# Performance work log

Hardware: AMD Instinct MI355X
Metric: run time of the kernel (lower is better)

The kernel has to match this reference:

```python
import jax, jax.numpy as jnp
import numpy as np

N_NODES, N_EDGES = 50000, 150000
HEADS, OUT = 2, 325


def _lin(k, i, o):
    return (jax.random.normal(k, (i, o), jnp.float32) / np.float32(np.sqrt(i)))


def setup_inputs() -> dict:
    key = jax.random.key(0)
    ks = jax.random.split(key, 24)
    h = jax.random.normal(ks[0], (N_NODES, 5), jnp.float32)
    edge_num = jax.random.normal(ks[1], (N_NODES, 5), jnp.float32)
    edge_index = jax.random.randint(ks[2], (2, N_EDGES), 0, N_NODES)
    edge_weight = jax.random.uniform(ks[3], (N_EDGES,), jnp.float32)
    d = dict(h=h, edge_num=edge_num, edge_index=edge_index, edge_weight=edge_weight)
    # five GCNConv layers: weight [5,64], bias [64]
    names = ['sum', 'mean', 'max', 'ne', 'nem']
    for i, nm in enumerate(names):
        d['W_' + nm] = _lin(ks[4 + i], 5, 64)
        d['b_' + nm] = jnp.zeros((64,), jnp.float32)
    # GATv2Conv params
    d['Wl'] = _lin(ks[10], 325, HEADS * OUT)
    d['Wr'] = _lin(ks[11], 325, HEADS * OUT)
    d['We'] = _lin(ks[12], 1, HEADS * OUT)
    d['att'] = jax.random.normal(ks[13], (HEADS, OUT), jnp.float32) / np.float32(np.sqrt(OUT))
    d['b_att'] = jnp.zeros((OUT,), jnp.float32)
    d['W_fc1'] = _lin(ks[14], 325, 5)
    d['b_fc1'] = jnp.zeros((5,), jnp.float32)
    return d


def _seg_mean(m, idx, n):
    s = jax.ops.segment_sum(m, idx, n)
    c = jax.ops.segment_sum(jnp.ones((m.shape[0],), m.dtype), idx, n)
    return s / jnp.clip(c, 1.0)[:, None]


def _seg_max0(m, idx, n):
    o = jax.ops.segment_max(m, idx, n)
    return jnp.where(jnp.isfinite(o), o, jnp.zeros_like(o))  # empty segments -> 0 (PyG behavior)


def _gcn(x, W, b, src, dst, w, aggr, n):
    # GCNConv(normalize=False, add_self_loops=False): aggr_j w_ij * (x_j @ W) + b
    m = (x @ W)[src]
    if w is not None:
        m = m * w[:, None]
    if aggr == 'add':
        o = jax.ops.segment_sum(m, dst, n)
    elif aggr == 'mean':
        o = _seg_mean(m, dst, n)
    else:
        o = _seg_max0(m, dst, n)
    return o + b


def _forward(h, edge_num, edge_weight, W_sum, b_sum, W_mean, b_mean, W_max, b_max,
             W_ne, b_ne, W_nem, b_nem, Wl, Wr, We, att, b_att, W_fc1, b_fc1, edge_index):
    n = h.shape[0]
    src, dst = edge_index[0], edge_index[1]
    h1 = _gcn(h, W_sum, b_sum, src, dst, edge_weight, 'add', n)
    h2 = _gcn(h, W_mean, b_mean, src, dst, edge_weight, 'mean', n)
    h3 = _gcn(h, W_max, b_max, src, dst, edge_weight, 'max', n)
    h4 = _gcn(h, W_ne, b_ne, src, dst, None, 'add', n)
    h5 = _gcn(h, W_nem, b_nem, src, dst, None, 'max', n)
    x = jnp.concatenate([h1, h2, h3, h4, h5, edge_num], axis=-1)  # [N, 325]
    # GATv2Conv(heads=2, concat=False, aggr='mean', add_self_loops=True, fill_value='mean')
    loop = jnp.arange(n)
    src2 = jnp.concatenate([src, loop])
    dst2 = jnp.concatenate([dst, loop])
    ea = jnp.concatenate([edge_weight[:, None], jnp.full((n, 1), jnp.mean(edge_weight))], axis=0)
    xl = (x @ Wl).reshape(n, HEADS, OUT)  # source transform
    xr = (x @ Wr).reshape(n, HEADS, OUT)  # target transform
    ee = (ea @ We).reshape(-1, HEADS, OUT)
    f = jax.nn.leaky_relu(xl[src2] + xr[dst2] + ee, 0.2)  # [E2, H, C]
    alpha = jnp.einsum('ehc,hc->eh', f, att)
    mx = jax.ops.segment_max(alpha, dst2, n)
    a = jnp.exp(alpha - mx[dst2])
    a = a / jax.ops.segment_sum(a, dst2, n)[dst2]  # softmax over incoming edges
    msg = xl[src2] * a[:, :, None]
    cnt = jax.ops.segment_sum(jnp.ones((src2.shape[0],), x.dtype), dst2, n)
    agg = jax.ops.segment_sum(msg, dst2, n) / jnp.clip(cnt, 1.0)[:, None, None]  # aggr='mean'
    o = agg.mean(axis=1) + b_att  # concat=False -> head mean
    return o @ W_fc1 + b_fc1


def reference(h, edge_num, edge_index, edge_weight, W_sum, b_sum, W_mean, b_mean,
              W_max, b_max, W_ne, b_ne, W_nem, b_nem, Wl, Wr, We, att, b_att,
              W_fc1, b_fc1):
    return _forward(h, edge_num, edge_weight, W_sum, b_sum, W_mean, b_mean, W_max, b_max,
                    W_ne, b_ne, W_nem, b_nem, Wl, Wr, We, att, b_att, W_fc1, b_fc1, edge_index)
```

## Files before the change

kernel.cpp:

```cpp
#include <hip/hip_runtime.h>
#include <hip/hip_bf16.h>
#include <math.h>

#define N_NODES 50000
#define N_EDGES 150000
#define FDIM 325
#define KP 352
#define HCP 1312
#define XROFF 656
#define LDA 40
#define LDC 136
#define NPAN 391
#define NBJ 11
#define SCAN_B 256
#define NBLK ((N_NODES + SCAN_B - 1) / SCAN_B)

typedef unsigned short ushort_t;
typedef __attribute__((ext_vector_type(8))) short short8v;
typedef __attribute__((ext_vector_type(4))) float f32x4;

__device__ __forceinline__ float bf2f(ushort_t u) {
  return __uint_as_float(((unsigned)u) << 16);
}
__device__ __forceinline__ ushort_t f2bf(float f) {
  __hip_bfloat16 h = __float2bfloat16(f);
  union { __hip_bfloat16 h; ushort_t u; } cv; cv.h = h;
  return cv.u;
}

__global__ void k_init(int* deg, int* cursor, float* red) {
  int i = blockIdx.x * blockDim.x + threadIdx.x;
  if (i < N_NODES) { deg[i] = 0; cursor[i] = 0; }
  if (i == 0) red[0] = 0.f;
}

__global__ void k_count(const int* __restrict__ dst, const float* __restrict__ ew,
                        int* deg, float* red) {
  int e = blockIdx.x * blockDim.x + threadIdx.x;
  float w = 0.f;
  if (e < N_EDGES) { atomicAdd(&deg[dst[e]], 1); w = ew[e]; }
  #pragma unroll
  for (int m = 32; m; m >>= 1) w += __shfl_xor(w, m);
  if ((threadIdx.x & 63) == 0) atomicAdd(red, w);
}

__global__ void k_scan1(const int* __restrict__ deg, int* offs, int* bsum) {
  __shared__ int buf[SCAN_B];
  int b = blockIdx.x, tid = threadIdx.x, i = b * SCAN_B + tid;
  int v = (i < N_NODES) ? deg[i] : 0;
  buf[tid] = v;
  __syncthreads();
  for (int o = 1; o < SCAN_B; o <<= 1) {
    int t = (tid >= o) ? buf[tid - o] : 0;
    __syncthreads();
    buf[tid] += t;
    __syncthreads();
  }
  if (i < N_NODES) offs[i + 1] = buf[tid];
  if (tid == SCAN_B - 1) bsum[b] = buf[tid];
}
__global__ void k_scan2(const int* __restrict__ bsum, int* bofs) {
  __shared__ int buf[256];
  int tid = threadIdx.x;
  int v = (tid < NBLK) ? bsum[tid] : 0;
  buf[tid] = v;
  __syncthreads();
  for (int o = 1; o < 256; o <<= 1) {
    int t = (tid >= o) ? buf[tid - o] : 0;
    __syncthreads();
    buf[tid] += t;
    __syncthreads();
  }
  if (tid < NBLK) bofs[tid] = buf[tid] - v;
}
__global__ void k_scan3(const int* __restrict__ bofs, int* offs) {
  int i = blockIdx.x * blockDim.x + threadIdx.x;
  if (i == 0) offs[0] = 0;
  if (i < N_NODES) offs[i + 1] += bofs[i / SCAN_B];
}

__global__ void k_scatter(const int* __restrict__ src, const int* __restrict__ dst,
                          const float* __restrict__ ew, const int* __restrict__ offs,
                          int* cursor, int* csr_src, float* csr_w) {
  int e = blockIdx.x * blockDim.x + threadIdx.x;
  if (e >= N_EDGES) return;
  int d = dst[e];
  int p = offs[d] + atomicAdd(&cursor[d], 1);
  csr_src[p] = src[e];
  csr_w[p] = ew[e];
}

__global__ void __launch_bounds__(64) k_gcn(
    const float* __restrict__ h, const float* __restrict__ edge_num,
    const int* __restrict__ offs, const int* __restrict__ csr_src,
    const float* __restrict__ csr_w,
    const float* __restrict__ Wsum, const float* __restrict__ bsum,
    const float* __restrict__ Wmean, const float* __restrict__ bmean,
    const float* __restrict__ Wmax, const float* __restrict__ bmax,
    const float* __restrict__ Wne, const float* __restrict__ bne,
    const float* __restrict__ Wnem, const float* __restrict__ bnem,
    ushort_t* __restrict__ x) {
  int n = blockIdx.x;
  int t = threadIdx.x;
  float w0[5], w1[5], w2[5], w3[5], w4[5];
  #pragma unroll
  for (int k = 0; k < 5; ++k) {
    w0[k] = Wsum[k * 64 + t];
    w1[k] = Wmean[k * 64 + t];
    w2[k] = Wmax[k * 64 + t];
    w3[k] = Wne[k * 64 + t];
    w4[k] = Wnem[k * 64 + t];
  }
  float s_sum = 0.f, s_wmean = 0.f, s_max = -INFINITY, s_ne = 0.f, s_nem = -INFINITY;
  int beg = offs[n], end = offs[n + 1];
  float wcur = 0.f, hcur[5];
  if (beg < end) {
    int s = csr_src[beg];
    wcur = csr_w[beg];
    #pragma unroll
    for (int k = 0; k < 5; ++k) hcur[k] = h[s * 5 + k];
  }
  for (int i = beg; i < end; ++i) {
    float wnxt = 0.f, hnxt[5];
    if (i + 1 < end) {
      int s = csr_src[i + 1];
      wnxt = csr_w[i + 1];
      #pragma unroll
      for (int k = 0; k < 5; ++k) hnxt[k] = h[s * 5 + k];
    }
    float v0 = 0, v1 = 0, v2 = 0, v3 = 0, v4 = 0;
    #pragma unroll
    for (int k = 0; k < 5; ++k) {
      v0 += hcur[k] * w0[k]; v1 += hcur[k] * w1[k]; v2 += hcur[k] * w2[k];
      v3 += hcur[k] * w3[k]; v4 += hcur[k] * w4[k];
    }
    s_sum += wcur * v0;
    s_wmean += wcur * v1;
    s_max = fmaxf(s_max, wcur * v2);
    s_ne += v3;
    s_nem = fmaxf(s_nem, v4);
    wcur = wnxt;
    #pragma unroll
    for (int k = 0; k < 5; ++k) hcur[k] = hnxt[k];
  }
  int dg = end - beg;
  float inv = 1.f / (float)(dg > 0 ? dg : 1);
  ushort_t* xr = x + (size_t)n * KP;
  xr[t]       = f2bf(s_sum + bsum[t]);
  xr[64 + t]  = f2bf(s_wmean * inv + bmean[t]);
  xr[128 + t] = f2bf((dg ? s_max : 0.f) + bmax[t]);
  xr[192 + t] = f2bf(s_ne + bne[t]);
  xr[256 + t] = f2bf((dg ? s_nem : 0.f) + bnem[t]);
  if (t < 5) xr[320 + t] = f2bf(edge_num[n * 5 + t]);
  if (t < KP - FDIM) xr[FDIM + t] = 0;
}

__global__ void k_wt(const float* __restrict__ Wl, const float* __restrict__ Wr,
                     ushort_t* __restrict__ Wt) {
  int t = blockIdx.x * blockDim.x + threadIdx.x;
  if (t >= HCP * KP) return;
  int n = t / KP, k = t % KP;
  float v = 0.f;
  if (k < FDIM) {
    if (n < 650) v = Wl[(size_t)k * 650 + n];
    else if (n >= XROFF && n < XROFF + 650) v = Wr[(size_t)k * 650 + (n - XROFF)];
  }
  Wt[t] = f2bf(v);
}

__global__ void __launch_bounds__(256) k_gemm_mfma(
    const ushort_t* __restrict__ x, const ushort_t* __restrict__ Wt,
    ushort_t* __restrict__ xlr) {
  __shared__ ushort_t smem[128 * LDA * 2];
  ushort_t* As = smem;
  ushort_t* Bs = smem + 128 * LDA;
  ushort_t* Cs = smem;

  int L = blockIdx.x;
  int panel, jb;
  if (L < 4224) {
    int chunk = L / 88, g = L % 88;
    panel = chunk * 8 + (g & 7);
    jb = g >> 3;
  } else {
    int g = L - 4224;
    panel = 384 + g % 7;
    jb = g / 7;
  }
  int bm = panel * 128, bn = jb * 128;

  int tid = threadIdx.x;
  int lane = tid & 63, wave = tid >> 6;
  int wr = wave >> 1, wc = wave & 1;
  int srow = tid >> 2, skc = (tid & 3) << 3;
  const float4 fz = make_float4(0.f, 0.f, 0.f, 0.f);

  float4 pa0, pa1, pb0, pb1;
  {
    int gm0 = bm + srow, gm1 = gm0 + 64;
    int gn0 = bn + srow, gn1 = gn0 + 64;
    pa0 = (gm0 < N_NODES) ? *(const float4*)&x[(size_t)gm0 * KP + skc] : fz;
    pa1 = (gm1 < N_NODES) ? *(const float4*)&x[(size_t)gm1 * KP + skc] : fz;
    pb0 = (gn0 < HCP)     ? *(const float4*)&Wt[(size_t)gn0 * KP + skc] : fz;
    pb1 = (gn1 < HCP)     ? *(const float4*)&Wt[(size_t)gn1 * KP + skc] : fz;
  }
  f32x4 acc[4][4] = {};
  for (int k0 = 0; k0 < KP; k0 += 32) {
    *(float4*)&As[srow * LDA + skc]        = pa0;
    *(float4*)&As[(srow + 64) * LDA + skc] = pa1;
    *(float4*)&Bs[srow * LDA + skc]        = pb0;
    *(float4*)&Bs[(srow + 64) * LDA + skc] = pb1;
    __syncthreads();
    int kn = k0 + 32;
    if (kn < KP) {
      int gm0 = bm + srow, gm1 = gm0 + 64;
      int gn0 = bn + srow, gn1 = gn0 + 64;
      pa0 = (gm0 < N_NODES) ? *(const float4*)&x[(size_t)gm0 * KP + kn + skc] : fz;
      pa1 = (gm1 < N_NODES) ? *(const float4*)&x[(size_t)gm1 * KP + kn + skc] : fz;
      pb0 = (gn0 < HCP)     ? *(const float4*)&Wt[(size_t)gn0 * KP + kn + skc] : fz;
      pb1 = (gn1 < HCP)     ? *(const float4*)&Wt[(size_t)gn1 * KP + kn + skc] : fz;
    }
    int koff = (lane >> 4) << 3;
    int ar = (wr << 6) + (lane & 15);
    int br = (wc << 6) + (lane & 15);
    short8v a[4], b[4];
    #pragma unroll
    for (int i = 0; i < 4; ++i) a[i] = *(const short8v*)&As[(ar + i * 16) * LDA + koff];
    #pragma unroll
    for (int j = 0; j < 4; ++j) b[j] = *(const short8v*)&Bs[(br + j * 16) * LDA + koff];
    #pragma unroll
    for (int i = 0; i < 4; ++i)
      #pragma unroll
      for (int j = 0; j < 4; ++j)
        acc[i][j] = __builtin_amdgcn_mfma_f32_16x16x32_bf16(a[i], b[j], acc[i][j], 0, 0, 0);
    __syncthreads();
  }
  #pragma unroll
  for (int half = 0; half < 2; ++half) {
    if (wr == half) {
      int lr0 = ((lane >> 4) << 2);
      int c0 = (wc << 6) + (lane & 15);
      #pragma unroll
      for (int i = 0; i < 4; ++i)
        #pragma unroll
        for (int j = 0; j < 4; ++j)
          #pragma unroll
          for (int r = 0; r < 4; ++r)
            Cs[(lr0 + i * 16 + r) * LDC + c0 + j * 16] = f2bf(acc[i][j][r]);
    }
    __syncthreads();
    #pragma unroll
    for (int it = 0; it < 4; ++it) {
      int idx = tid + it * 256;
      int lr = idx >> 4, cc = idx & 15;
      int row = bm + half * 64 + lr;
      int col = bn + cc * 8;
      if (row < N_NODES && col < HCP) {
        short8v v = *(const short8v*)&Cs[lr * LDC + cc * 8];
        *(short8v*)&xlr[(size_t)row * HCP + col] = v;
      }
    }
    __syncthreads();
  }
}

__global__ void k_wlf(const float* __restrict__ Wl, const float* __restrict__ Wfc,
                      float* __restrict__ Wlf) {
  int t = blockIdx.x * blockDim.x + threadIdx.x;
  if (t >= FDIM * 10) return;
  int cp = t / 10, o = t % 10;
  int hh = o / 5, j = o % 5;
  float s = 0.f;
  for (int c = 0; c < 325; ++c) s += Wl[(size_t)cp * 650 + hh * 325 + c] * Wfc[c * 5 + j];
  Wlf[cp * 10 + o] = s;
}

__global__ void k_yl(const ushort_t* __restrict__ x, const float* __restrict__ Wlf,
                     float* __restrict__ yl) {
  int wid = (blockIdx.x * blockDim.x + threadIdx.x) >> 6;
  int lane = threadIdx.x & 63;
  if (wid >= N_NODES) return;
  const ushort_t* row = x + (size_t)wid * KP;
  float p[10] = {};
  for (int c = lane; c < FDIM; c += 64) {
    float v = bf2f(row[c]);
    const float* wr = Wlf + c * 10;
    #pragma unroll
    for (int j = 0; j < 10; ++j) p[j] += v * wr[j];
  }
  #pragma unroll
  for (int j = 0; j < 10; ++j)
    #pragma unroll
    for (int m = 32; m; m >>= 1) p[j] += __shfl_xor(p[j], m);
  if (lane == 0) {
    #pragma unroll
    for (int j = 0; j < 10; ++j) yl[(size_t)wid * 10 + j] = p[j];
  }
}

__global__ void k_cvec(const float* __restrict__ b_att, const float* __restrict__ Wfc,
                       const float* __restrict__ b_fc1, const float* __restrict__ red,
                       float* __restrict__ cvec) {
  int j = threadIdx.x;
  if (j == 5) cvec[5] = red[0] / (float)N_EDGES;
  if (j < 5) {
    float s = b_fc1[j];
    for (int c = 0; c < 325; ++c) s += b_att[c] * Wfc[c * 5 + j];
    cvec[j] = s;
  }
}

__global__ void __launch_bounds__(64) k_att(
    const int* __restrict__ offs, const int* __restrict__ csrs,
    const float* __restrict__ csrw, const ushort_t* __restrict__ xlr,
    const float* __restrict__ We, const float* __restrict__ att,
    const float* __restrict__ cvec, const float* __restrict__ yl,
    float* __restrict__ out) {
  int d = blockIdx.x;
  int lane = threadIdx.x;
  float xd0[8], xd1[8], We0[8], We1[8], at0[8], at1[8];
  const ushort_t* xd = xlr + (size_t)d * HCP + XROFF;
  {
    short8v v = *(const short8v*)&xd[lane * 8];
    int c0 = lane * 8;
    #pragma unroll
    for (int e = 0; e < 8; ++e) {
      xd0[e] = bf2f((ushort_t)v[e]);
      We0[e] = We[c0 + e];
      at0[e] = att[c0 + e];
    }
  }
  if (lane < 18) {
    short8v v = *(const short8v*)&xd[512 + lane * 8];
    int c0 = 512 + lane * 8;
    #pragma unroll
    for (int e = 0; e < 8; ++e) {
      bool ok = (c0 + e) < 650;
      xd1[e] = bf2f((ushort_t)v[e]);
      We1[e] = ok ? We[c0 + e] : 0.f;
      at1[e] = ok ? att[c0 + e] : 0.f;
    }
  }
  float meanw = cvec[5];
  int beg = offs[d], end = offs[d + 1];
  float m0 = -INFINITY, m1 = -INFINITY, s0 = 0.f, s1 = 0.f;
  float oj = 0.f;

  float ea_c, yv_c = 0.f;
  short8v v0_c, v1_c;
  {
    int s;
    if (beg < end) { s = csrs[beg]; ea_c = csrw[beg]; }
    else { s = d; ea_c = meanw; }
    const ushort_t* xs = xlr + (size_t)s * HCP;
    v0_c = *(const short8v*)&xs[lane * 8];
    if (lane < 18) v1_c = *(const short8v*)&xs[512 + lane * 8];
    if (lane < 10) yv_c = yl[(size_t)s * 10 + lane];
  }
  for (int i = beg; i <= end; ++i) {
    float ea_n = 0.f, yv_n = 0.f;
    short8v v0_n, v1_n;
    bool have_next = (i < end);
    if (have_next) {
      int s;
      if (i + 1 < end) { s = csrs[i + 1]; ea_n = csrw[i + 1]; }
      else { s = d; ea_n = meanw; }
      const ushort_t* xs = xlr + (size_t)s * HCP;
      v0_n = *(const short8v*)&xs[lane * 8];
      if (lane < 18) v1_n = *(const short8v*)&xs[512 + lane * 8];
      if (lane < 10) yv_n = yl[(size_t)s * 10 + lane];
    }
    float p0 = 0.f, p1 = 0.f;
    {
      int c0 = lane * 8;
      #pragma unroll
      for (int e = 0; e < 8; ++e) {
        float vv = bf2f((ushort_t)v0_c[e]) + xd0[e] + ea_c * We0[e];
        vv = (vv > 0.f) ? vv : 0.2f * vv;
        float t = vv * at0[e];
        if (c0 + e < 325) p0 += t; else p1 += t;
      }
    }
    if (lane < 18) {
      #pragma unroll
      for (int e = 0; e < 8; ++e) {
        float vv = bf2f((ushort_t)v1_c[e]) + xd1[e] + ea_c * We1[e];
        vv = (vv > 0.f) ? vv : 0.2f * vv;
        p1 += vv * at1[e];
      }
    }
    #pragma unroll
    for (int m = 32; m; m >>= 1) { p0 += __shfl_xor(p0, m); p1 += __shfl_xor(p1, m); }
    float nm0 = fmaxf(m0, p0), nm1 = fmaxf(m1, p1);
    float r0 = __expf(m0 - nm0), r1 = __expf(m1 - nm1);
    float e0 = __expf(p0 - nm0), e1 = __expf(p1 - nm1);
    s0 = s0 * r0 + e0; s1 = s1 * r1 + e1;
    m0 = nm0; m1 = nm1;
    if (lane < 10) {
      float r = (lane < 5) ? r0 : r1;
      float e = (lane < 5) ? e0 : e1;
      oj = oj * r + e * yv_c;
    }
    if (have_next) { ea_c = ea_n; yv_c = yv_n; v0_c = v0_n; v1_c = v1_n; }
  }
  float on = oj / ((lane < 5) ? s0 : s1);
  float other = __shfl(on, lane + 5);
  if (lane < 5) {
    int dg = end - beg;
    out[(size_t)d * 5 + lane] = (on + other) / (2.f * (float)(dg + 1)) + cvec[lane];
  }
}

extern "C" void kernel_launch(void* const* d_in, const int* in_sizes, int n_in,
                              void* d_out, int out_size, void* d_ws, size_t ws_size,
                              hipStream_t stream) {
  (void)in_sizes; (void)n_in; (void)out_size; (void)ws_size;
  const float* h        = (const float*)d_in[0];
  const float* edge_num = (const float*)d_in[1];
  const int*   eidx     = (const int*)d_in[2];
  const float* ew       = (const float*)d_in[3];
  const float* Wsum  = (const float*)d_in[4];  const float* bsum_  = (const float*)d_in[5];
  const float* Wmean = (const float*)d_in[6];  const float* bmean = (const float*)d_in[7];
  const float* Wmax  = (const float*)d_in[8];  const float* bmax  = (const float*)d_in[9];
  const float* Wne   = (const float*)d_in[10]; const float* bne   = (const float*)d_in[11];
  const float* Wnem  = (const float*)d_in[12]; const float* bnem  = (const float*)d_in[13];
  const float* Wl    = (const float*)d_in[14]; const float* Wr    = (const float*)d_in[15];
  const float* We    = (const float*)d_in[16]; const float* att   = (const float*)d_in[17];
  const float* b_att = (const float*)d_in[18];
  const float* Wfc   = (const float*)d_in[19]; const float* bfc   = (const float*)d_in[20];
  const int* src = eidx;
  const int* dst = eidx + N_EDGES;
  float* out = (float*)d_out;

  char* p = (char*)d_ws;
  size_t off = 0;
  auto alloc = [&](size_t bytes) { char* r = p + off; off = (off + bytes + 255) & ~(size_t)255; return r; };
  ushort_t* x   = (ushort_t*)alloc((size_t)N_NODES * KP * 2);
  ushort_t* xlr = (ushort_t*)alloc((size_t)N_NODES * HCP * 2);
  ushort_t* Wt  = (ushort_t*)alloc((size_t)HCP * KP * 2);
  float* yl     = (float*)alloc((size_t)N_NODES * 10 * 4);
  int*   deg    = (int*)alloc((size_t)N_NODES * 4);
  int*   offs   = (int*)alloc((size_t)(N_NODES + 1) * 4);
  int*   cursor = (int*)alloc((size_t)N_NODES * 4);
  int*   csrs   = (int*)alloc((size_t)N_EDGES * 4);
  float* csrw   = (float*)alloc((size_t)N_EDGES * 4);
  int*   bsum   = (int*)alloc((size_t)NBLK * 4);
  int*   bofs   = (int*)alloc((size_t)NBLK * 4);
  float* Wlf    = (float*)alloc((size_t)FDIM * 10 * 4);
  float* red    = (float*)alloc(64);
  float* cvec   = (float*)alloc(64);

  k_init<<<(N_NODES + 255) / 256, 256, 0, stream>>>(deg, cursor, red);
  k_count<<<(N_EDGES + 255) / 256, 256, 0, stream>>>(dst, ew, deg, red);
  k_scan1<<<NBLK, SCAN_B, 0, stream>>>(deg, offs, bsum);
  k_scan2<<<1, 256, 0, stream>>>(bsum, bofs);
  k_scan3<<<NBLK, SCAN_B, 0, stream>>>(bofs, offs);
  k_scatter<<<(N_EDGES + 255) / 256, 256, 0, stream>>>(src, dst, ew, offs, cursor, csrs, csrw);
  k_gcn<<<N_NODES, 64, 0, stream>>>(h, edge_num, offs, csrs, csrw,
                                    Wsum, bsum_, Wmean, bmean, Wmax, bmax,
                                    Wne, bne, Wnem, bnem, x);
  k_wt<<<(HCP * KP + 255) / 256, 256, 0, stream>>>(Wl, Wr, Wt);
  k_gemm_mfma<<<NPAN * NBJ, 256, 0, stream>>>(x, Wt, xlr);
  k_wlf<<<(FDIM * 10 + 255) / 256, 256, 0, stream>>>(Wl, Wfc, Wlf);
  k_yl<<<(N_NODES * 64 + 255) / 256, 256, 0, stream>>>(x, Wlf, yl);
  k_cvec<<<1, 64, 0, stream>>>(b_att, Wfc, bfc, red, cvec);
  k_att<<<N_NODES, 64, 0, stream>>>(offs, csrs, csrw, xlr, We, att, cvec, yl, out);
}
```

Baseline: 410.4 us.

## Use persistent waves with atomic work counter for GCN and attention kernels

Replaces the one-block-per-node launches of the GCN aggregation and GATv2 attention kernels with a fixed grid of 256-thread blocks. Each wavefront repeatedly claims a destination node through a global atomic counter. Per-wave constants (weights, biases, attention vectors) are now loaded once and reused across many nodes. This is meant to cut block launch/scheduling overhead and balance degree skew, at the cost of one atomic per node and two extra counters to reset.

```diff
diff --git a/kernel.cpp b/kernel.cpp
--- a/kernel.cpp
+++ b/kernel.cpp
@@ -28,10 +28,10 @@
   return cv.u;
 }
 
-__global__ void k_init(int* deg, int* cursor, float* red) {
+__global__ void k_init(int* deg, int* cursor, float* red, int* wc1, int* wc2) {
   int i = blockIdx.x * blockDim.x + threadIdx.x;
   if (i < N_NODES) { deg[i] = 0; cursor[i] = 0; }
-  if (i == 0) red[0] = 0.f;
+  if (i == 0) { red[0] = 0.f; wc1[0] = 0; wc2[0] = 0; }
 }
 
 __global__ void k_count(const int* __restrict__ dst, const float* __restrict__ ew,
@@ -90,7 +90,7 @@
   csr_w[p] = ew[e];
 }
 
-__global__ void __launch_bounds__(64) k_gcn(
+__global__ void __launch_bounds__(256) k_gcn(
     const float* __restrict__ h, const float* __restrict__ edge_num,
     const int* __restrict__ offs, const int* __restrict__ csr_src,
     const float* __restrict__ csr_w,
@@ -99,9 +99,8 @@
     const float* __restrict__ Wmax, const float* __restrict__ bmax,
     const float* __restrict__ Wne, const float* __restrict__ bne,
     const float* __restrict__ Wnem, const float* __restrict__ bnem,
-    ushort_t* __restrict__ x) {
-  int n = blockIdx.x;
-  int t = threadIdx.x;
+    ushort_t* __restrict__ x, int* __restrict__ workc) {
+  int t = threadIdx.x & 63;
   float w0[5], w1[5], w2[5], w3[5], w4[5];
   #pragma unroll
   for (int k = 0; k < 5; ++k) {
@@ -111,48 +110,55 @@
     w3[k] = Wne[k * 64 + t];
     w4[k] = Wnem[k * 64 + t];
   }
-  float s_sum = 0.f, s_wmean = 0.f, s_max = -INFINITY, s_ne = 0.f, s_nem = -INFINITY;
-  int beg = offs[n], end = offs[n + 1];
-  float wcur = 0.f, hcur[5];
-  if (beg < end) {
-    int s = csr_src[beg];
-    wcur = csr_w[beg];
-    #pragma unroll
-    for (int k = 0; k < 5; ++k) hcur[k] = h[s * 5 + k];
-  }
-  for (int i = beg; i < end; ++i) {
-    float wnxt = 0.f, hnxt[5];
-    if (i + 1 < end) {
-      int s = csr_src[i + 1];
-      wnxt = csr_w[i + 1];
-      #pragma unroll
-      for (int k = 0; k < 5; ++k) hnxt[k] = h[s * 5 + k];
-    }
-    float v0 = 0, v1 = 0, v2 = 0, v3 = 0, v4 = 0;
-    #pragma unroll
-    for (int k = 0; k < 5; ++k) {
-      v0 += hcur[k] * w0[k]; v1 += hcur[k] * w1[k]; v2 += hcur[k] * w2[k];
-      v3 += hcur[k] * w3[k]; v4 += hcur[k] * w4[k];
-    }
-    s_sum += wcur * v0;
-    s_wmean += wcur * v1;
-    s_max = fmaxf(s_max, wcur * v2);
-    s_ne += v3;
-    s_nem = fmaxf(s_nem, v4);
-    wcur = wnxt;
-    #pragma unroll
-    for (int k = 0; k < 5; ++k) hcur[k] = hnxt[k];
-  }
-  int dg = end - beg;
-  float inv = 1.f / (float)(dg > 0 ? dg : 1);
-  ushort_t* xr = x + (size_t)n * KP;
-  xr[t]       = f2bf(s_sum + bsum[t]);
-  xr[64 + t]  = f2bf(s_wmean * inv + bmean[t]);
-  xr[128 + t] = f2bf((dg ? s_max : 0.f) + bmax[t]);
-  xr[192 + t] = f2bf(s_ne + bne[t]);
-  xr[256 + t] = f2bf((dg ? s_nem : 0.f) + bnem[t]);
-  if (t < 5) xr[320 + t] = f2bf(edge_num[n * 5 + t]);
-  if (t < KP - FDIM) xr[FDIM + t] = 0;
+  float b0 = bsum[t], b1 = bmean[t], b2 = bmax[t], b3 = bne[t], b4 = bnem[t];
+  for (;;) {
+    int n;
+    if (t == 0) n = atomicAdd(workc, 1);
+    n = __shfl(n, 0);
+    if (n >= N_NODES) break;
+    float s_sum = 0.f, s_wmean = 0.f, s_max = -INFINITY, s_ne = 0.f, s_nem = -INFINITY;
+    int beg = offs[n], end = offs[n + 1];
+    float wcur = 0.f, hcur[5];
+    if (beg < end) {
+      int s = csr_src[beg];
+      wcur = csr_w[beg];
+      #pragma unroll
+      for (int k = 0; k < 5; ++k) hcur[k] = h[s * 5 + k];
+    }
+    for (int i = beg; i < end; ++i) {
+      float wnxt = 0.f, hnxt[5];
+      if (i + 1 < end) {
+        int s = csr_src[i + 1];
+        wnxt = csr_w[i + 1];
+        #pragma unroll
+        for (int k = 0; k < 5; ++k) hnxt[k] = h[s * 5 + k];
+      }
+      float v0 = 0, v1 = 0, v2 = 0, v3 = 0, v4 = 0;
+      #pragma unroll
+      for (int k = 0; k < 5; ++k) {
+        v0 += hcur[k] * w0[k]; v1 += hcur[k] * w1[k]; v2 += hcur[k] * w2[k];
+        v3 += hcur[k] * w3[k]; v4 += hcur[k] * w4[k];
+      }
+      s_sum += wcur * v0;
+      s_wmean += wcur * v1;
+      s_max = fmaxf(s_max, wcur * v2);
+      s_ne += v3;
+      s_nem = fmaxf(s_nem, v4);
+      wcur = wnxt;
+      #pragma unroll
+      for (int k = 0; k < 5; ++k) hcur[k] = hnxt[k];
+    }
+    int dg = end - beg;
+    float inv = 1.f / (float)(dg > 0 ? dg : 1);
+    ushort_t* xr = x + (size_t)n * KP;
+    xr[t]       = f2bf(s_sum + b0);
+    xr[64 + t]  = f2bf(s_wmean * inv + b1);
+    xr[128 + t] = f2bf((dg ? s_max : 0.f) + b2);
+    xr[192 + t] = f2bf(s_ne + b3);
+    xr[256 + t] = f2bf((dg ? s_nem : 0.f) + b4);
+    if (t < 5) xr[320 + t] = f2bf(edge_num[n * 5 + t]);
+    if (t < KP - FDIM) xr[FDIM + t] = 0;
+  }
 }
 
 __global__ void k_wt(const float* __restrict__ Wl, const float* __restrict__ Wr,
@@ -310,104 +316,116 @@
   }
 }
 
-__global__ void __launch_bounds__(64) k_att(
+__global__ void __launch_bounds__(256) k_att(
     const int* __restrict__ offs, const int* __restrict__ csrs,
     const float* __restrict__ csrw, const ushort_t* __restrict__ xlr,
     const float* __restrict__ We, const float* __restrict__ att,
     const float* __restrict__ cvec, const float* __restrict__ yl,
-    float* __restrict__ out) {
-  int d = blockIdx.x;
-  int lane = threadIdx.x;
-  float xd0[8], xd1[8], We0[8], We1[8], at0[8], at1[8];
-  const ushort_t* xd = xlr + (size_t)d * HCP + XROFF;
+    float* __restrict__ out, int* __restrict__ workc) {
+  int lane = threadIdx.x & 63;
+  float We0[8], We1[8], at0[8], at1[8];
   {
-    short8v v = *(const short8v*)&xd[lane * 8];
     int c0 = lane * 8;
     #pragma unroll
-    for (int e = 0; e < 8; ++e) {
-      xd0[e] = bf2f((ushort_t)v[e]);
-      We0[e] = We[c0 + e];
-      at0[e] = att[c0 + e];
-    }
+    for (int e = 0; e < 8; ++e) { We0[e] = We[c0 + e]; at0[e] = att[c0 + e]; }
   }
   if (lane < 18) {
-    short8v v = *(const short8v*)&xd[512 + lane * 8];
     int c0 = 512 + lane * 8;
     #pragma unroll
     for (int e = 0; e < 8; ++e) {
       bool ok = (c0 + e) < 650;
-      xd1[e] = bf2f((ushort_t)v[e]);
       We1[e] = ok ? We[c0 + e] : 0.f;
       at1[e] = ok ? att[c0 + e] : 0.f;
     }
   }
   float meanw = cvec[5];
-  int beg = offs[d], end = offs[d + 1];
-  float m0 = -INFINITY, m1 = -INFINITY, s0 = 0.f, s1 = 0.f;
-  float oj = 0.f;
-
-  float ea_c, yv_c = 0.f;
-  short8v v0_c, v1_c;
-  {
-    int s;
-    if (beg < end) { s = csrs[beg]; ea_c = csrw[beg]; }
-    else { s = d; ea_c = meanw; }
-    const ushort_t* xs = xlr + (size_t)s * HCP;
-    v0_c = *(const short8v*)&xs[lane * 8];
-    if (lane < 18) v1_c = *(const short8v*)&xs[512 + lane * 8];
-    if (lane < 10) yv_c = yl[(size_t)s * 10 + lane];
-  }
-  for (int i = beg; i <= end; ++i) {
-    float ea_n = 0.f, yv_n = 0.f;
-    short8v v0_n, v1_n;
-    bool have_next = (i < end);
-    if (have_next) {
+  float cv = (lane < 5) ? cvec[lane] : 0.f;
+
+  for (;;) {
+    int d;
+    if (lane == 0) d = atomicAdd(workc, 1);
+    d = __shfl(d, 0);
+    if (d >= N_NODES) break;
+
+    float xd0[8], xd1[8];
+    const ushort_t* xd = xlr + (size_t)d * HCP + XROFF;
+    {
+      short8v v = *(const short8v*)&xd[lane * 8];
+      #pragma unroll
+      for (int e = 0; e < 8; ++e) xd0[e] = bf2f((ushort_t)v[e]);
+    }
+    if (lane < 18) {
+      short8v v = *(const short8v*)&xd[512 + lane * 8];
+      #pragma unroll
+      for (int e = 0; e < 8; ++e) xd1[e] = bf2f((ushort_t)v[e]);
+    }
+    int beg = offs[d], end = offs[d + 1];
+    float m0 = -INFINITY, m1 = -INFINITY, s0 = 0.f, s1 = 0.f;
+    float oj = 0.f;
+
+    float ea_c, yv_c = 0.f;
+    short8v v0_c, v1_c;
+    {
       int s;
-      if (i + 1 < end) { s = csrs[i + 1]; ea_n = csrw[i + 1]; }
-      else { s = d; ea_n = meanw; }
+      if (beg < end) { s = csrs[beg]; ea_c = csrw[beg]; }
+      else { s = d; ea_c = meanw; }
       const ushort_t* xs = xlr + (size_t)s * HCP;
-      v0_n = *(const short8v*)&xs[lane * 8];
-      if (lane < 18) v1_n = *(const short8v*)&xs[512 + lane * 8];
-      if (lane < 10) yv_n = yl[(size_t)s * 10 + lane];
-    }
-    float p0 = 0.f, p1 = 0.f;
-    {
-      int c0 = lane * 8;
-      #pragma unroll
-      for (int e = 0; e < 8; ++e) {
-        float vv = bf2f((ushort_t)v0_c[e]) + xd0[e] + ea_c * We0[e];
-        vv = (vv > 0.f) ? vv : 0.2f * vv;
-        float t = vv * at0[e];
-        if (c0 + e < 325) p0 += t; else p1 += t;
-      }
-    }
-    if (lane < 18) {
-      #pragma unroll
-      for (int e = 0; e < 8; ++e) {
-        float vv = bf2f((ushort_t)v1_c[e]) + xd1[e] + ea_c * We1[e];
-        vv = (vv > 0.f) ? vv : 0.2f * vv;
-        p1 += vv * at1[e];
-      }
-    }
-    #pragma unroll
-    for (int m = 32; m; m >>= 1) { p0 += __shfl_xor(p0, m); p1 += __shfl_xor(p1, m); }
-    float nm0 = fmaxf(m0, p0), nm1 = fmaxf(m1, p1);
-    float r0 = __expf(m0 - nm0), r1 = __expf(m1 - nm1);
-    float e0 = __expf(p0 - nm0), e1 = __expf(p1 - nm1);
-    s0 = s0 * r0 + e0; s1 = s1 * r1 + e1;
-    m0 = nm0; m1 = nm1;
-    if (lane < 10) {
-      float r = (lane < 5) ? r0 : r1;
-      float e = (lane < 5) ? e0 : e1;
-      oj = oj * r + e * yv_c;
-    }
-    if (have_next) { ea_c = ea_n; yv_c = yv_n; v0_c = v0_n; v1_c = v1_n; }
-  }
-  float on = oj / ((lane < 5) ? s0 : s1);
-  float other = __shfl(on, lane + 5);
-  if (lane < 5) {
-    int dg = end - beg;
-    out[(size_t)d * 5 + lane] = (on + other) / (2.f * (float)(dg + 1)) + cvec[lane];
+      v0_c = *(const short8v*)&xs[lane * 8];
+      if (lane < 18) v1_c = *(const short8v*)&xs[512 + lane * 8];
+      if (lane < 10) yv_c = yl[(size_t)s * 10 + lane];
+    }
+    for (int i = beg; i <= end; ++i) {
+      float ea_n = 0.f, yv_n = 0.f;
+      short8v v0_n, v1_n;
+      bool have_next = (i < end);
+      if (have_next) {
+        int s;
+        if (i + 1 < end) { s = csrs[i + 1]; ea_n = csrw[i + 1]; }
+        else { s = d; ea_n = meanw; }
+        const ushort_t* xs = xlr + (size_t)s * HCP;
+        v0_n = *(const short8v*)&xs[lane * 8];
+        if (lane < 18) v1_n = *(const short8v*)&xs[512 + lane * 8];
+        if (lane < 10) yv_n = yl[(size_t)s * 10 + lane];
+      }
+      float p0 = 0.f, p1 = 0.f;
+      {
+        int c0 = lane * 8;
+        #pragma unroll
+        for (int e = 0; e < 8; ++e) {
+          float vv = bf2f((ushort_t)v0_c[e]) + xd0[e] + ea_c * We0[e];
+          vv = (vv > 0.f) ? vv : 0.2f * vv;
+          float t = vv * at0[e];
+          if (c0 + e < 325) p0 += t; else p1 += t;
+        }
+      }
+      if (lane < 18) {
+        #pragma unroll
+        for (int e = 0; e < 8; ++e) {
+          float vv = bf2f((ushort_t)v1_c[e]) + xd1[e] + ea_c * We1[e];
+          vv = (vv > 0.f) ? vv : 0.2f * vv;
+          p1 += vv * at1[e];
+        }
+      }
+      #pragma unroll
+      for (int m = 32; m; m >>= 1) { p0 += __shfl_xor(p0, m); p1 += __shfl_xor(p1, m); }
+      float nm0 = fmaxf(m0, p0), nm1 = fmaxf(m1, p1);
+      float r0 = __expf(m0 - nm0), r1 = __expf(m1 - nm1);
+      float e0 = __expf(p0 - nm0), e1 = __expf(p1 - nm1);
+      s0 = s0 * r0 + e0; s1 = s1 * r1 + e1;
+      m0 = nm0; m1 = nm1;
+      if (lane < 10) {
+        float r = (lane < 5) ? r0 : r1;
+        float e = (lane < 5) ? e0 : e1;
+        oj = oj * r + e * yv_c;
+      }
+      if (have_next) { ea_c = ea_n; yv_c = yv_n; v0_c = v0_n; v1_c = v1_n; }
+    }
+    float on = oj / ((lane < 5) ? s0 : s1);
+    float other = __shfl(on, lane + 5);
+    if (lane < 5) {
+      int dg = end - beg;
+      out[(size_t)d * 5 + lane] = (on + other) / (2.f * (float)(dg + 1)) + cv;
+    }
   }
 }
 
@@ -449,20 +467,22 @@
   float* Wlf    = (float*)alloc((size_t)FDIM * 10 * 4);
   float* red    = (float*)alloc(64);
   float* cvec   = (float*)alloc(64);
-
-  k_init<<<(N_NODES + 255) / 256, 256, 0, stream>>>(deg, cursor, red);
+  int*   wc1    = (int*)alloc(64);
+  int*   wc2    = (int*)alloc(64);
+
+  k_init<<<(N_NODES + 255) / 256, 256, 0, stream>>>(deg, cursor, red, wc1, wc2);
   k_count<<<(N_EDGES + 255) / 256, 256, 0, stream>>>(dst, ew, deg, red);
   k_scan1<<<NBLK, SCAN_B, 0, stream>>>(deg, offs, bsum);
   k_scan2<<<1, 256, 0, stream>>>(bsum, bofs);
   k_scan3<<<NBLK, SCAN_B, 0, stream>>>(bofs, offs);
   k_scatter<<<(N_EDGES + 255) / 256, 256, 0, stream>>>(src, dst, ew, offs, cursor, csrs, csrw);
-  k_gcn<<<N_NODES, 64, 0, stream>>>(h, edge_num, offs, csrs, csrw,
-                                    Wsum, bsum_, Wmean, bmean, Wmax, bmax,
-                                    Wne, bne, Wnem, bnem, x);
+  k_gcn<<<2048, 256, 0, stream>>>(h, edge_num, offs, csrs, csrw,
+                                  Wsum, bsum_, Wmean, bmean, Wmax, bmax,
+                                  Wne, bne, Wnem, bnem, x, wc1);
   k_wt<<<(HCP * KP + 255) / 256, 256, 0, stream>>>(Wl, Wr, Wt);
   k_gemm_mfma<<<NPAN * NBJ, 256, 0, stream>>>(x, Wt, xlr);
   k_wlf<<<(FDIM * 10 + 255) / 256, 256, 0, stream>>>(Wl, Wfc, Wlf);
   k_yl<<<(N_NODES * 64 + 255) / 256, 256, 0, stream>>>(x, Wlf, yl);
   k_cvec<<<1, 64, 0, stream>>>(b_att, Wfc, bfc, red, cvec);
-  k_att<<<N_NODES, 64, 0, stream>>>(offs, csrs, csrw, xlr, We, att, cvec, yl, out);
-}
+  k_att<<<2048, 256, 0, stream>>>(offs, csrs, csrw, xlr, We, att, cvec, yl, out, wc2);
+}
```

Result: slower. 1.636 ms (+298.6%).
